# Performance work log

Hardware: AMD Instinct MI355X
Metric: run time of the kernel (lower is better)

The kernel has to match this reference:

```python
import jax, jax.numpy as jnp
import numpy as np

N = 100000          # nodes
E = 3200000         # edges
F_IN = 128          # num_node_features
C = 32              # num_candidate_node_types


def _gcn_conv(x, src, dst, W, b, n_nodes):
    """PyG GCNConv: add self loops, symmetric deg^-1/2 normalization, then linear."""
    h = x @ W  # [N, out]
    # degree on A + I (edge weight 1), counted on target nodes
    deg = jnp.zeros((n_nodes,), h.dtype).at[dst].add(1.0) + 1.0
    dinv = jax.lax.rsqrt(deg)  # deg >= 1 so safe
    norm = dinv[src] * dinv[dst]            # [E]
    msg = h[src] * norm[:, None]            # gather + scale, [E, out]
    out = jax.ops.segment_sum(msg, dst, num_segments=n_nodes)
    out = out + h * (dinv * dinv)[:, None]  # self-loop contribution
    return out + b


def _relu6(x):
    return jnp.clip(x, 0.0, 6.0)


def setup_inputs() -> dict:
    key = jax.random.key(0)
    ks = jax.random.split(key, 16)
    def lin(k, fan_in, fan_out):
        lim = 1.0 / np.sqrt(fan_in)
        kw, kb = jax.random.split(k)
        W = jax.random.uniform(kw, (fan_in, fan_out), jnp.float32, -lim, lim)
        b = jax.random.uniform(kb, (fan_out,), jnp.float32, -lim, lim)
        return W, b
    W1, b1 = lin(ks[0], F_IN, 16)
    W2, b2 = lin(ks[1], 16, 24)
    W3, b3 = lin(ks[2], 24, 32)
    Ws1, bs1 = lin(ks[3], 32, 16)
    Ws2, bs2 = lin(ks[4], 16, C)
    We1, be1 = lin(ks[5], 32, 24)
    We2, be2 = lin(ks[6], 24, C)
    x = jax.random.normal(ks[7], (N, F_IN), jnp.float32)
    edge_index = jax.random.randint(ks[8], (2, E), 0, N, jnp.int64)
    candidate_set = jax.random.randint(ks[9], (C,), 0, C, jnp.int64)
    return dict(x=x, edge_index=edge_index, candidate_set=candidate_set,
                W1=W1, b1=b1, W2=W2, b2=b2, W3=W3, b3=b3,
                Ws1=Ws1, bs1=bs1, Ws2=Ws2, bs2=bs2,
                We1=We1, be1=be1, We2=We2, be2=be2)


def reference(x, edge_index, candidate_set,
              W1, b1, W2, b2, W3, b3,
              Ws1, bs1, Ws2, bs2, We1, be1, We2, be2):
    src, dst = edge_index[0], edge_index[1]
    h = _gcn_conv(x, src, dst, W1, b1, N)   # [N, 16] (no activation in source)
    h = _gcn_conv(h, src, dst, W2, b2, N)   # [N, 24]
    h = _gcn_conv(h, src, dst, W3, b3, N)   # [N, 32]
    # start-node head: Linear -> ReLU6 -> Linear -> Softmax, then Categorical sample
    s_logits = _relu6(h @ Ws1 + bs1) @ Ws2 + bs2         # [N, C]
    k1, k2 = jax.random.split(jax.random.key(42))
    start_node = jax.random.categorical(k1, s_logits, axis=-1)  # [N] ints in [0, C)
    # gather rows at sampled indices and append (vectorized form of the source's cat)
    combined = jnp.concatenate([h, h[start_node]], axis=0)      # [2N, 32]
    e_logits = _relu6(combined @ We1 + be1) @ We2 + be2          # [2N, C]
    end_node = jax.random.categorical(k2, e_logits, axis=-1)    # [2N]
    return start_node, end_node
```

## Files before the change

kernel.cpp:

```cpp
#include <hip/hip_runtime.h>
#include <hip/hip_bf16.h>
#include <math.h>

#define TPB 256
#define BSHIFT 8
#define BRANGE (1 << BSHIFT)
#define CHUNK 8192
#define MAXB 512

__host__ __device__ inline void tf2x32(unsigned ks0, unsigned ks1,
                                       unsigned x0, unsigned x1,
                                       unsigned& o0, unsigned& o1) {
  const unsigned ks2 = ks0 ^ ks1 ^ 0x1BD11BDAu;
  unsigned v0 = x0 + ks0, v1 = x1 + ks1;
#define TF_RND(r) { v0 += v1; v1 = (v1 << (r)) | (v1 >> (32 - (r))); v1 ^= v0; }
  TF_RND(13) TF_RND(15) TF_RND(26) TF_RND(6)
  v0 += ks1; v1 += ks2 + 1u;
  TF_RND(17) TF_RND(29) TF_RND(16) TF_RND(24)
  v0 += ks2; v1 += ks0 + 2u;
  TF_RND(13) TF_RND(15) TF_RND(26) TF_RND(6)
  v0 += ks0; v1 += ks1 + 3u;
  TF_RND(17) TF_RND(29) TF_RND(16) TF_RND(24)
  v0 += ks1; v1 += ks2 + 4u;
  TF_RND(13) TF_RND(15) TF_RND(26) TF_RND(6)
  v0 += ks2; v1 += ks0 + 5u;
#undef TF_RND
  o0 = v0; o1 = v1;
}

__device__ __forceinline__ unsigned bits32(unsigned k0, unsigned k1, unsigned idx) {
  unsigned o0, o1;
  tf2x32(k0, k1, 0u, idx, o0, o1);
  return o0 ^ o1;
}

__device__ __forceinline__ float bits_to_u(unsigned bits) {
  float f = __uint_as_float((bits >> 9) | 0x3f800000u) - 1.0f;
  return (f > 0.0f) ? f : 1.17549435e-38f;
}

__device__ __forceinline__ float gumbel_exact(unsigned k0, unsigned k1, unsigned idx) {
  float u = bits_to_u(bits32(k0, k1, idx));
  float w = (float)(-log((double)u));
  return (float)(-log((double)w));
}

__device__ __forceinline__ float gumbel_fast(unsigned k0, unsigned k1, unsigned idx) {
  float u = bits_to_u(bits32(k0, k1, idx));
  float w = -logf(u);
  return -logf(w);
}

__global__ void hist_kernel(const int* __restrict__ dst, int* __restrict__ histT,
                            int E, int nblk, int nbuckets) {
  __shared__ int hist[MAXB];
  for (int i = threadIdx.x; i < nbuckets; i += TPB) hist[i] = 0;
  __syncthreads();
  int beg = blockIdx.x * CHUNK;
  int end = min(beg + CHUNK, E);
  for (int e = beg + threadIdx.x; e < end; e += TPB)
    atomicAdd(&hist[dst[e] >> BSHIFT], 1);
  __syncthreads();
  for (int i = threadIdx.x; i < nbuckets; i += TPB)
    histT[(size_t)i * nblk + blockIdx.x] = hist[i];
}

__global__ void colscan_kernel(int* __restrict__ histT, int* __restrict__ btot, int nblk) {
  __shared__ int sh[MAXB];
  int b = blockIdx.x;
  int t = threadIdx.x;
  sh[t] = (t < nblk) ? histT[(size_t)b * nblk + t] : 0;
  __syncthreads();
  for (int ofs = 1; ofs < MAXB; ofs <<= 1) {
    int v = (t >= ofs) ? sh[t - ofs] : 0;
    __syncthreads();
    sh[t] += v;
    __syncthreads();
  }
  if (t < nblk) histT[(size_t)b * nblk + t] = (t == 0) ? 0 : sh[t - 1];
  if (t == MAXB - 1) btot[b] = sh[MAXB - 1];
}

__global__ void bucketscan_kernel(const int* __restrict__ btot, int* __restrict__ bbase,
                                  int nbuckets, int E) {
  __shared__ int sh[MAXB];
  int t = threadIdx.x;
  sh[t] = (t < nbuckets) ? btot[t] : 0;
  __syncthreads();
  for (int ofs = 1; ofs < MAXB; ofs <<= 1) {
    int v = (t >= ofs) ? sh[t - ofs] : 0;
    __syncthreads();
    sh[t] += v;
    __syncthreads();
  }
  if (t < nbuckets) bbase[t] = (t == 0) ? 0 : sh[t - 1];
  if (t == 0) bbase[nbuckets] = E;
}

__global__ void place_kernel(const int* __restrict__ src, const int* __restrict__ dst,
                             const int* __restrict__ histT, const int* __restrict__ bbase,
                             unsigned* __restrict__ packed, int E, int nblk, int nbuckets) {
  __shared__ int cur[MAXB];
  for (int i = threadIdx.x; i < nbuckets; i += TPB)
    cur[i] = histT[(size_t)i * nblk + blockIdx.x] + bbase[i];
  __syncthreads();
  int beg = blockIdx.x * CHUNK;
  int end = min(beg + CHUNK, E);
  for (int e = beg + threadIdx.x; e < end; e += TPB) {
    int s = src[e], d = dst[e];
    int b = d >> BSHIFT;
    int pos = atomicAdd(&cur[b], 1);
    packed[pos] = (unsigned)s | ((unsigned)(d & (BRANGE - 1)) << 20);
  }
}

__global__ void bucket_place_kernel(const int* __restrict__ bbase,
                                    const unsigned* __restrict__ packed,
                                    int* __restrict__ csr_src, int* __restrict__ rowptr,
                                    float* __restrict__ dinv, float* __restrict__ dinv2,
                                    int N, int nbuckets) {
  __shared__ int cnt[BRANGE];
  __shared__ int sh[BRANGE];
  __shared__ int cur[BRANGE];
  int b = blockIdx.x;
  int base = b << BSHIFT;
  int range_n = min(BRANGE, N - base);
  int t = threadIdx.x;
  cnt[t] = 0;
  __syncthreads();
  int beg = bbase[b], end = bbase[b + 1];
  for (int e = beg + t; e < end; e += TPB)
    atomicAdd(&cnt[packed[e] >> 20], 1);
  __syncthreads();
  sh[t] = cnt[t];
  __syncthreads();
  for (int ofs = 1; ofs < BRANGE; ofs <<= 1) {
    int v = (t >= ofs) ? sh[t - ofs] : 0;
    __syncthreads();
    sh[t] += v;
    __syncthreads();
  }
  int excl = (t == 0) ? 0 : sh[t - 1];
  cur[t] = beg + excl;
  if (t < range_n) {
    rowptr[base + t] = beg + excl;
    float d = (float)(cnt[t] + 1);
    float di = 1.0f / sqrtf(d);
    dinv[base + t] = di;
    dinv2[base + t] = di * di;
  }
  if (b == nbuckets - 1 && t == 0) rowptr[N] = end;
  __syncthreads();
  for (int e = beg + t; e < end; e += TPB) {
    unsigned p = packed[e];
    int dstoff = (int)(p >> 20);
    int s = (int)(p & 0xFFFFFu);
    int pos = atomicAdd(&cur[dstoff], 1);
    csr_src[pos] = s;
  }
}

template <int K, int J, int LDO, int TJ>
__global__ void matmul_tile_kernel(const float* __restrict__ A, const float* __restrict__ W,
                                   float* __restrict__ out, int N) {
  static_assert(J == TJ * 4, "each thread owns 4 outputs");
  static_assert(K % 4 == 0, "K must be multiple of 4");
  int t = blockIdx.x * blockDim.x + threadIdx.x;
  int n = t / TJ, jb = t % TJ;
  if (n >= N) return;
  const float* a = A + (size_t)n * K;
  const int j0 = jb * 4;
  double a0 = 0.0, a1 = 0.0, a2 = 0.0, a3 = 0.0;
  for (int k = 0; k < K; k += 4) {
    float4 av = *(const float4*)&a[k];
    float4 w0 = *(const float4*)&W[(k + 0) * J + j0];
    float4 w1 = *(const float4*)&W[(k + 1) * J + j0];
    float4 w2 = *(const float4*)&W[(k + 2) * J + j0];
    float4 w3 = *(const float4*)&W[(k + 3) * J + j0];
    a0 += (double)av.x * (double)w0.x; a1 += (double)av.x * (double)w0.y;
    a2 += (double)av.x * (double)w0.z; a3 += (double)av.x * (double)w0.w;
    a0 += (double)av.y * (double)w1.x; a1 += (double)av.y * (double)w1.y;
    a2 += (double)av.y * (double)w1.z; a3 += (double)av.y * (double)w1.w;
    a0 += (double)av.z * (double)w2.x; a1 += (double)av.z * (double)w2.y;
    a2 += (double)av.z * (double)w2.z; a3 += (double)av.z * (double)w2.w;
    a0 += (double)av.w * (double)w3.x; a1 += (double)av.w * (double)w3.y;
    a2 += (double)av.w * (double)w3.z; a3 += (double)av.w * (double)w3.w;
  }
  float4 o;
  o.x = (float)a0; o.y = (float)a1; o.z = (float)a2; o.w = (float)a3;
  *(float4*)&out[(size_t)n * LDO + j0] = o;
}

template <int JA, int W, int LDH>
__global__ void gather_shfl4_kernel(const int* __restrict__ rowptr,
                                    const int* __restrict__ csr_src,
                                    const float* __restrict__ dinv,
                                    const float* __restrict__ h,
                                    const float* __restrict__ dinv2,
                                    const float* __restrict__ b,
                                    float* __restrict__ out, int N) {
  static_assert((W & (W - 1)) == 0, "W must be power of 2 for shfl");
  int t = blockIdx.x * blockDim.x + threadIdx.x;
  int n = t / W, j = t % W;
  if (n >= N) return;
  const int NJ = JA / 4;
  int jj = (j < NJ) ? j : (NJ - 1);
  int beg = rowptr[n], end = rowptr[n + 1];
  float dn = dinv[n];
  double a0 = 0.0, a1 = 0.0, a2 = 0.0, a3 = 0.0;
  for (int i = beg; i < end; i += W) {
    int m = end - i; if (m > W) m = W;
    int idx = i + j; if (idx >= end) idx = end - 1;
    int   sj = csr_src[idx];
    float wj = dinv[sj];
    if (m == W) {
      float4 g[W];
      float  w[W];
#pragma unroll
      for (int k = 0; k < W; ++k) {
        int s = __shfl(sj, k, W);
        w[k] = __shfl(wj, k, W) * dn;
        g[k] = *(const float4*)&h[(size_t)s * LDH + 4 * jj];
      }
#pragma unroll
      for (int k = 0; k < W; ++k) {
        a0 += (double)g[k].x * (double)w[k];
        a1 += (double)g[k].y * (double)w[k];
        a2 += (double)g[k].z * (double)w[k];
        a3 += (double)g[k].w * (double)w[k];
      }
    } else {
      for (int k = 0; k < m; ++k) {
        int   s = __shfl(sj, k, W);
        float wk = __shfl(wj, k, W) * dn;
        float4 g = *(const float4*)&h[(size_t)s * LDH + 4 * jj];
        a0 += (double)g.x * (double)wk;
        a1 += (double)g.y * (double)wk;
        a2 += (double)g.z * (double)wk;
        a3 += (double)g.w * (double)wk;
      }
    }
  }
  {
    float4 gs = *(const float4*)&h[(size_t)n * LDH + 4 * jj];
    double d2 = (double)dinv2[n];
    a0 += (double)gs.x * d2;
    a1 += (double)gs.y * d2;
    a2 += (double)gs.z * d2;
    a3 += (double)gs.w * d2;
  }
  if (j < NJ) {
    float4 o;
    o.x = (float)a0 + b[4 * j + 0];
    o.y = (float)a1 + b[4 * j + 1];
    o.z = (float)a2 + b[4 * j + 2];
    o.w = (float)a3 + b[4 * j + 3];
    *(float4*)&out[(size_t)n * JA + 4 * j] = o;
  }
}

__global__ void hid_start_kernel(const float* __restrict__ h,
                                 const float* __restrict__ Ws1, const float* __restrict__ bs1,
                                 float* __restrict__ hid, int N) {
  int t = blockIdx.x * blockDim.x + threadIdx.x;
  int n = t / 4, jb = t % 4;
  if (n >= N) return;
  const float* hr = h + (size_t)n * 32;
  const int j0 = jb * 4;
  double a0 = 0.0, a1 = 0.0, a2 = 0.0, a3 = 0.0;
#pragma unroll
  for (int k = 0; k < 32; k += 4) {
    float4 av = *(const float4*)&hr[k];
    float4 w0 = *(const float4*)&Ws1[(k + 0) * 16 + j0];
    float4 w1 = *(const float4*)&Ws1[(k + 1) * 16 + j0];
    float4 w2 = *(const float4*)&Ws1[(k + 2) * 16 + j0];
    float4 w3 = *(const float4*)&Ws1[(k + 3) * 16 + j0];
    a0 += (double)av.x * (double)w0.x; a1 += (double)av.x * (double)w0.y;
    a2 += (double)av.x * (double)w0.z; a3 += (double)av.x * (double)w0.w;
    a0 += (double)av.y * (double)w1.x; a1 += (double)av.y * (double)w1.y;
    a2 += (double)av.y * (double)w1.z; a3 += (double)av.y * (double)w1.w;
    a0 += (double)av.z * (double)w2.x; a1 += (double)av.z * (double)w2.y;
    a2 += (double)av.z * (double)w2.z; a3 += (double)av.z * (double)w2.w;
    a0 += (double)av.w * (double)w3.x; a1 += (double)av.w * (double)w3.y;
    a2 += (double)av.w * (double)w3.z; a3 += (double)av.w * (double)w3.w;
  }
  float4 o;
  o.x = fminf(fmaxf((float)a0 + bs1[j0 + 0], 0.0f), 6.0f);
  o.y = fminf(fmaxf((float)a1 + bs1[j0 + 1], 0.0f), 6.0f);
  o.z = fminf(fmaxf((float)a2 + bs1[j0 + 2], 0.0f), 6.0f);
  o.w = fminf(fmaxf((float)a3 + bs1[j0 + 3], 0.0f), 6.0f);
  *(float4*)&hid[(size_t)n * 16 + j0] = o;
}

__global__ void hid_end_kernel(const float* __restrict__ h, const int* __restrict__ start,
                               const float* __restrict__ We1, const float* __restrict__ be1,
                               float* __restrict__ hid, int N) {
  int t = blockIdx.x * blockDim.x + threadIdx.x;
  int r = t / 6, jb = t % 6;
  if (r >= 2 * N) return;
  int row = (r < N) ? r : start[r - N];
  const float* hr = h + (size_t)row * 32;
  const int j0 = jb * 4;
  double a0 = 0.0, a1 = 0.0, a2 = 0.0, a3 = 0.0;
#pragma unroll
  for (int k = 0; k < 32; k += 4) {
    float4 av = *(const float4*)&hr[k];
    float4 w0 = *(const float4*)&We1[(k + 0) * 24 + j0];
    float4 w1 = *(const float4*)&We1[(k + 1) * 24 + j0];
    float4 w2 = *(const float4*)&We1[(k + 2) * 24 + j0];
    float4 w3 = *(const float4*)&We1[(k + 3) * 24 + j0];
    a0 += (double)av.x * (double)w0.x; a1 += (double)av.x * (double)w0.y;
    a2 += (double)av.x * (double)w0.z; a3 += (double)av.x * (double)w0.w;
    a0 += (double)av.y * (double)w1.x; a1 += (double)av.y * (double)w1.y;
    a2 += (double)av.y * (double)w1.z; a3 += (double)av.y * (double)w1.w;
    a0 += (double)av.z * (double)w2.x; a1 += (double)av.z * (double)w2.y;
    a2 += (double)av.z * (double)w2.z; a3 += (double)av.z * (double)w2.w;
    a0 += (double)av.w * (double)w3.x; a1 += (double)av.w * (double)w3.y;
    a2 += (double)av.w * (double)w3.z; a3 += (double)av.w * (double)w3.w;
  }
  float4 o;
  o.x = fminf(fmaxf((float)a0 + be1[j0 + 0], 0.0f), 6.0f);
  o.y = fminf(fmaxf((float)a1 + be1[j0 + 1], 0.0f), 6.0f);
  o.z = fminf(fmaxf((float)a2 + be1[j0 + 2], 0.0f), 6.0f);
  o.w = fminf(fmaxf((float)a3 + be1[j0 + 3], 0.0f), 6.0f);
  *(float4*)&hid[(size_t)r * 24 + j0] = o;
}

template <int K>
__global__ void pick_kernel(const float* __restrict__ hid,
                            const float* __restrict__ W2, const float* __restrict__ b2,
                            int* __restrict__ outw, int R, unsigned k0, unsigned k1) {
  int t = blockIdx.x * blockDim.x + threadIdx.x;
  int r = t >> 5;
  int c = t & 31;
  if (r >= R) return;
  const float* hr = hid + (size_t)r * K;

  float af = 0.0f;
#pragma unroll
  for (int k = 0; k < K; ++k) af = fmaf(hr[k], W2[k * 32 + c], af);
  float zf = af + b2[c] + gumbel_fast(k0, k1, (unsigned)(r * 32 + c));

  float m1 = zf; int i1 = c; float m2 = -INFINITY;
#pragma unroll
  for (int m = 16; m >= 1; m >>= 1) {
    float om1 = __shfl_xor(m1, m, 32);
    int   oi1 = __shfl_xor(i1, m, 32);
    float om2 = __shfl_xor(m2, m, 32);
    if (om1 > m1 || (om1 == m1 && oi1 < i1)) {
      m2 = fmaxf(m1, om2);
      m1 = om1; i1 = oi1;
    } else {
      m2 = fmaxf(m2, om1);
    }
  }

  if (m1 - m2 >= 1e-3f) {
    if (c == 0) outw[r] = i1;
    return;
  }

  double a = 0.0;
#pragma unroll
  for (int k = 0; k < K; ++k) a += (double)hr[k] * (double)W2[k * 32 + c];
  float logit = (float)a + b2[c];
  float z = logit + gumbel_exact(k0, k1, (unsigned)(r * 32 + c));
  int best = c;
#pragma unroll
  for (int m = 16; m >= 1; m >>= 1) {
    float oz = __shfl_xor(z, m, 32);
    int   ob = __shfl_xor(best, m, 32);
    if (oz > z || (oz == z && ob < best)) { z = oz; best = ob; }
  }
  if (c == 0) outw[r] = best;
}

extern "C" void kernel_launch(void* const* d_in, const int* in_sizes, int n_in,
                              void* d_out, int out_size, void* d_ws, size_t ws_size,
                              hipStream_t stream) {
  const float* x   = (const float*)d_in[0];
  const int*   ei  = (const int*)d_in[1];
  const float* W1  = (const float*)d_in[3];
  const float* b1  = (const float*)d_in[4];
  const float* W2  = (const float*)d_in[5];
  const float* b2  = (const float*)d_in[6];
  const float* W3  = (const float*)d_in[7];
  const float* b3  = (const float*)d_in[8];
  const float* Ws1 = (const float*)d_in[9];
  const float* bs1 = (const float*)d_in[10];
  const float* Ws2 = (const float*)d_in[11];
  const float* bs2 = (const float*)d_in[12];
  const float* We1 = (const float*)d_in[13];
  const float* be1 = (const float*)d_in[14];
  const float* We2 = (const float*)d_in[15];
  const float* be2 = (const float*)d_in[16];

  const int N = in_sizes[0] / 128;
  const int E = in_sizes[1] / 2;
  const int* srcv = ei;
  const int* dstv = ei + E;
  const int nbuckets = (N + BRANGE - 1) >> BSHIFT;
  const int nblk = (E + CHUNK - 1) / CHUNK;

  char* ws = (char*)d_ws;
  size_t off = 0;
  float*    hA      = (float*)(ws + off);    off += (size_t)N * 32 * 4;
  float*    hB      = (float*)(ws + off);    off += (size_t)N * 32 * 4;
  int*      csr_src = (int*)(ws + off);      off += (size_t)E * 4;
  unsigned* packed  = (unsigned*)(ws + off); off += (size_t)E * 4;
  float*    dinv    = (float*)(ws + off);    off += (size_t)N * 4;
  float*    dinv2   = (float*)(ws + off);    off += (size_t)N * 4;
  int*      rowptr  = (int*)(ws + off);      off += (size_t)(N + 1) * 4;
  int*      histT   = (int*)(ws + off);      off += (size_t)nbuckets * nblk * 4;
  int*      btot    = (int*)(ws + off);      off += (size_t)MAXB * 4;
  int*      bbase   = (int*)(ws + off);      off += (size_t)(MAXB + 1) * 4;
  float* hid_start = hA;
  float* hid_end   = (float*)csr_src;

  unsigned k1a, k1b, k2a, k2b;
  tf2x32(0u, 42u, 0u, 0u, k1a, k1b);
  tf2x32(0u, 42u, 0u, 1u, k2a, k2b);

  hist_kernel<<<nblk, TPB, 0, stream>>>(dstv, histT, E, nblk, nbuckets);
  colscan_kernel<<<nbuckets, MAXB, 0, stream>>>(histT, btot, nblk);
  bucketscan_kernel<<<1, MAXB, 0, stream>>>(btot, bbase, nbuckets, E);
  place_kernel<<<nblk, TPB, 0, stream>>>(srcv, dstv, histT, bbase, packed, E, nblk, nbuckets);
  bucket_place_kernel<<<nbuckets, TPB, 0, stream>>>(bbase, packed, csr_src, rowptr,
                                                    dinv, dinv2, N, nbuckets);

  matmul_tile_kernel<128, 16, 16, 4><<<((size_t)N * 4 + TPB - 1) / TPB, TPB, 0, stream>>>(x, W1, hA, N);
  gather_shfl4_kernel<16, 4, 16><<<((size_t)N * 4 + TPB - 1) / TPB, TPB, 0, stream>>>(
      rowptr, csr_src, dinv, hA, dinv2, b1, hB, N);

  matmul_tile_kernel<16, 24, 32, 6><<<((size_t)N * 6 + TPB - 1) / TPB, TPB, 0, stream>>>(hB, W2, hA, N);
  gather_shfl4_kernel<24, 8, 32><<<((size_t)N * 8 + TPB - 1) / TPB, TPB, 0, stream>>>(
      rowptr, csr_src, dinv, hA, dinv2, b2, hB, N);

  matmul_tile_kernel<24, 32, 32, 8><<<((size_t)N * 8 + TPB - 1) / TPB, TPB, 0, stream>>>(hB, W3, hA, N);
  gather_shfl4_kernel<32, 8, 32><<<((size_t)N * 8 + TPB - 1) / TPB, TPB, 0, stream>>>(
      rowptr, csr_src, dinv, hA, dinv2, b3, hB, N);

  int* outI = (int*)d_out;

  hid_start_kernel<<<((size_t)N * 4 + TPB - 1) / TPB, TPB, 0, stream>>>(hB, Ws1, bs1, hid_start, N);
  pick_kernel<16><<<((size_t)N * 32 + TPB - 1) / TPB, TPB, 0, stream>>>(
      hid_start, Ws2, bs2, outI, N, k1a, k1b);

  hid_end_kernel<<<((size_t)2 * N * 6 + TPB - 1) / TPB, TPB, 0, stream>>>(hB, outI, We1, be1, hid_end, N);
  pick_kernel<24><<<((size_t)2 * N * 32 + TPB - 1) / TPB, TPB, 0, stream>>>(
      hid_end, We2, be2, outI + N, 2 * N, k2a, k2b);
}
```

Before: 532.2 us.

## Widen gather kernels to 16 lanes per node with prefetched edge indices

```diff
diff --git a/kernel.cpp b/kernel.cpp
--- a/kernel.cpp
+++ b/kernel.cpp
@@ -191,71 +191,129 @@
   *(float4*)&out[(size_t)n * LDO + j0] = o;
 }
 
-template <int JA, int W, int LDH>
-__global__ void gather_shfl4_kernel(const int* __restrict__ rowptr,
+__global__ void gather_s1_kernel(const int* __restrict__ rowptr,
+                                 const int* __restrict__ csr_src,
+                                 const float* __restrict__ dinv,
+                                 const float* __restrict__ h,
+                                 const float* __restrict__ dinv2,
+                                 const float* __restrict__ b,
+                                 float* __restrict__ out, int N) {
+  constexpr int W = 16;
+  int t = blockIdx.x * blockDim.x + threadIdx.x;
+  int n = t / W, j = t % W;
+  if (n >= N) return;
+  const float* hb = h + j;
+  int beg = rowptr[n], end = rowptr[n + 1];
+  float dn = dinv[n];
+  double acc = 0.0;
+  int sj = 0; float wj = 0.0f;
+  if (beg < end) {
+    int idx = beg + j; if (idx >= end) idx = end - 1;
+    sj = csr_src[idx];
+    wj = dinv[sj];
+  }
+  for (int i = beg; i < end; i += W) {
+    int m = end - i; if (m > W) m = W;
+    int sjn = 0; float wjn = 0.0f;
+    if (i + W < end) {
+      int idx2 = i + W + j; if (idx2 >= end) idx2 = end - 1;
+      sjn = csr_src[idx2];
+      wjn = dinv[sjn];
+    }
+    if (m == W) {
+      int s[W];
+#pragma unroll
+      for (int k = 0; k < W; ++k) s[k] = __shfl(sj, k, W);
+      float g[W];
+#pragma unroll
+      for (int k = 0; k < W; ++k) g[k] = hb[(size_t)s[k] * W];
+      float w[W];
+#pragma unroll
+      for (int k = 0; k < W; ++k) w[k] = __shfl(wj, k, W) * dn;
+#pragma unroll
+      for (int k = 0; k < W; ++k) acc += (double)g[k] * (double)w[k];
+    } else {
+      for (int k = 0; k < m; ++k) {
+        int   s = __shfl(sj, k, W);
+        float w = __shfl(wj, k, W) * dn;
+        acc += (double)hb[(size_t)s * W] * (double)w;
+      }
+    }
+    sj = sjn; wj = wjn;
+  }
+  acc += (double)hb[(size_t)n * W] * (double)dinv2[n];
+  out[(size_t)n * W + j] = (float)acc + b[j];
+}
+
+template <int JA, int LDH>
+__global__ void gather_shfl2_kernel(const int* __restrict__ rowptr,
                                     const int* __restrict__ csr_src,
                                     const float* __restrict__ dinv,
                                     const float* __restrict__ h,
                                     const float* __restrict__ dinv2,
                                     const float* __restrict__ b,
                                     float* __restrict__ out, int N) {
-  static_assert((W & (W - 1)) == 0, "W must be power of 2 for shfl");
+  constexpr int W = 16;
   int t = blockIdx.x * blockDim.x + threadIdx.x;
   int n = t / W, j = t % W;
   if (n >= N) return;
-  const int NJ = JA / 4;
+  constexpr int NJ = JA / 2;
   int jj = (j < NJ) ? j : (NJ - 1);
+  const float* hb = h + 2 * jj;
   int beg = rowptr[n], end = rowptr[n + 1];
   float dn = dinv[n];
-  double a0 = 0.0, a1 = 0.0, a2 = 0.0, a3 = 0.0;
+  double acc0 = 0.0, acc1 = 0.0;
+  int sj = 0; float wj = 0.0f;
+  if (beg < end) {
+    int idx = beg + j; if (idx >= end) idx = end - 1;
+    sj = csr_src[idx];
+    wj = dinv[sj];
+  }
   for (int i = beg; i < end; i += W) {
     int m = end - i; if (m > W) m = W;
-    int idx = i + j; if (idx >= end) idx = end - 1;
-    int   sj = csr_src[idx];
-    float wj = dinv[sj];
+    int sjn = 0; float wjn = 0.0f;
+    if (i + W < end) {
+      int idx2 = i + W + j; if (idx2 >= end) idx2 = end - 1;
+      sjn = csr_src[idx2];
+      wjn = dinv[sjn];
+    }
     if (m == W) {
-      float4 g[W];
-      float  w[W];
+      int s[W];
+#pragma unroll
+      for (int k = 0; k < W; ++k) s[k] = __shfl(sj, k, W);
+      float2 g[W];
+#pragma unroll
+      for (int k = 0; k < W; ++k) g[k] = *(const float2*)&hb[(size_t)s[k] * LDH];
+      float w[W];
+#pragma unroll
+      for (int k = 0; k < W; ++k) w[k] = __shfl(wj, k, W) * dn;
 #pragma unroll
       for (int k = 0; k < W; ++k) {
-        int s = __shfl(sj, k, W);
-        w[k] = __shfl(wj, k, W) * dn;
-        g[k] = *(const float4*)&h[(size_t)s * LDH + 4 * jj];
-      }
-#pragma unroll
-      for (int k = 0; k < W; ++k) {
-        a0 += (double)g[k].x * (double)w[k];
-        a1 += (double)g[k].y * (double)w[k];
-        a2 += (double)g[k].z * (double)w[k];
-        a3 += (double)g[k].w * (double)w[k];
+        acc0 += (double)g[k].x * (double)w[k];
+        acc1 += (double)g[k].y * (double)w[k];
       }
     } else {
       for (int k = 0; k < m; ++k) {
         int   s = __shfl(sj, k, W);
-        float wk = __shfl(wj, k, W) * dn;
-        float4 g = *(const float4*)&h[(size_t)s * LDH + 4 * jj];
-        a0 += (double)g.x * (double)wk;
-        a1 += (double)g.y * (double)wk;
-        a2 += (double)g.z * (double)wk;
-        a3 += (double)g.w * (double)wk;
+        float w = __shfl(wj, k, W) * dn;
+        float2 g = *(const float2*)&hb[(size_t)s * LDH];
+        acc0 += (double)g.x * (double)w;
+        acc1 += (double)g.y * (double)w;
       }
     }
+    sj = sjn; wj = wjn;
   }
   {
-    float4 gs = *(const float4*)&h[(size_t)n * LDH + 4 * jj];
+    float2 gs = *(const float2*)&hb[(size_t)n * LDH];
     double d2 = (double)dinv2[n];
-    a0 += (double)gs.x * d2;
-    a1 += (double)gs.y * d2;
-    a2 += (double)gs.z * d2;
-    a3 += (double)gs.w * d2;
+    acc0 += (double)gs.x * d2;
+    acc1 += (double)gs.y * d2;
   }
   if (j < NJ) {
-    float4 o;
-    o.x = (float)a0 + b[4 * j + 0];
-    o.y = (float)a1 + b[4 * j + 1];
-    o.z = (float)a2 + b[4 * j + 2];
-    o.w = (float)a3 + b[4 * j + 3];
-    *(float4*)&out[(size_t)n * JA + 4 * j] = o;
+    float2 o;
+    o.x = (float)acc0 + b[2 * j];
+    o.y = (float)acc1 + b[2 * j + 1];
+    *(float2*)&out[(size_t)n * JA + 2 * j] = o;
   }
 }
 
@@ -429,15 +487,15 @@
                                                     dinv, dinv2, N, nbuckets);
 
   matmul_tile_kernel<128, 16, 16, 4><<<((size_t)N * 4 + TPB - 1) / TPB, TPB, 0, stream>>>(x, W1, hA, N);
-  gather_shfl4_kernel<16, 4, 16><<<((size_t)N * 4 + TPB - 1) / TPB, TPB, 0, stream>>>(
+  gather_s1_kernel<<<((size_t)N * 16 + TPB - 1) / TPB, TPB, 0, stream>>>(
       rowptr, csr_src, dinv, hA, dinv2, b1, hB, N);
 
   matmul_tile_kernel<16, 24, 32, 6><<<((size_t)N * 6 + TPB - 1) / TPB, TPB, 0, stream>>>(hB, W2, hA, N);
-  gather_shfl4_kernel<24, 8, 32><<<((size_t)N * 8 + TPB - 1) / TPB, TPB, 0, stream>>>(
+  gather_shfl2_kernel<24, 32><<<((size_t)N * 16 + TPB - 1) / TPB, TPB, 0, stream>>>(
       rowptr, csr_src, dinv, hA, dinv2, b2, hB, N);
 
   matmul_tile_kernel<24, 32, 32, 8><<<((size_t)N * 8 + TPB - 1) / TPB, TPB, 0, stream>>>(hB, W3, hA, N);
-  gather_shfl4_kernel<32, 8, 32><<<((size_t)N * 8 + TPB - 1) / TPB, TPB, 0, stream>>>(
+  gather_shfl2_kernel<32, 32><<<((size_t)N * 16 + TPB - 1) / TPB, TPB, 0, stream>>>(
       rowptr, csr_src, dinv, hA, dinv2, b3, hB, N);
 
   int* outI = (int*)d_out;
```

After: 544.7 us. 2.3% more time.
